# Kernel tuning notes

Hardware: AMD Instinct MI355X
Metric: run time of the kernel (lower is better)

Reference implementation:

```python
import jax, jax.numpy as jnp
import numpy as np

B, S, E, NH = 2, 2048, 1024, 4
DH = E // NH
EPS = 1e-6  # backend stabilization eps and layernorm eps


def setup_inputs() -> dict:
    key = jax.random.key(0)
    ks = jax.random.split(key, 7)
    q = jax.random.normal(ks[0], (B, S, E), jnp.float32)
    k = jax.random.normal(ks[1], (B, S, E), jnp.float32)
    v = jax.random.normal(ks[2], (B, S, E), jnp.float32)
    # Gate Dense layers: kernel zero-init in the module; use small random so the
    # math is non-trivial. Biases follow the module's inits.
    igate_kernel = 0.02 * jax.random.normal(ks[3], (3 * E, NH), jnp.float32)
    fgate_kernel = 0.02 * jax.random.normal(ks[4], (3 * E, NH), jnp.float32)
    igate_bias = 0.1 * jax.random.normal(ks[5], (NH,), jnp.float32)
    fgate_bias = jnp.linspace(3.0, 6.0, NH, dtype=jnp.float32)  # bias_linspace_init(3,6)
    outnorm_weight = jnp.ones((NH, DH), jnp.float32)
    return {
        "q": q, "k": k, "v": v,
        "igate_kernel": igate_kernel, "igate_bias": igate_bias,
        "fgate_kernel": fgate_kernel, "fgate_bias": fgate_bias,
        "outnorm_weight": outnorm_weight,
    }


def _mlstm_parallel_stabilized(q, k, v, ig, fg):
    # q,k,v: (B,NH,S,DH); ig,fg: (B,NH,S) gate pre-activations
    log_fg = jax.nn.log_sigmoid(fg)                     # (B,NH,S)
    c = jnp.cumsum(log_fg, axis=-1)                     # cumulative forget gates
    # log decay matrix: entry (i,j) = sum_{s=j+1..i} log_fg[s] = c[i]-c[j], causal
    log_fg_mat = c[..., :, None] - c[..., None, :]      # (B,NH,S,S)
    causal = jnp.tril(jnp.ones((S, S), bool))
    log_D = jnp.where(causal, log_fg_mat + ig[..., None, :], -jnp.inf)
    max_log_D = jnp.max(log_D, axis=-1, keepdims=True)  # (B,NH,S,1)
    D = jnp.exp(log_D - max_log_D)                      # stabilized decay matrix
    qk = jnp.einsum("bhsd,bhtd->bhst", q, k) / jnp.sqrt(jnp.float32(DH))
    C = qk * D                                          # (B,NH,S,S)
    normalizer = jnp.maximum(jnp.abs(jnp.sum(C, axis=-1, keepdims=True)),
                             jnp.exp(-max_log_D))
    C_norm = C / (normalizer + EPS)
    return jnp.einsum("bhst,bhtd->bhsd", C_norm, v)     # (B,NH,S,DH)


def reference(q, k, v, igate_kernel, igate_bias, fgate_kernel, fgate_bias, outnorm_weight):
    gate_in = jnp.concatenate([q, k, v], axis=-1)       # (B,S,3E)
    ig = gate_in @ igate_kernel + igate_bias            # (B,S,NH)
    fg = gate_in @ fgate_kernel + fgate_bias            # (B,S,NH)
    qh = q.reshape(B, S, NH, DH).transpose(0, 2, 1, 3)  # (B,NH,S,DH)
    kh = k.reshape(B, S, NH, DH).transpose(0, 2, 1, 3)
    vh = v.reshape(B, S, NH, DH).transpose(0, 2, 1, 3)
    h = _mlstm_parallel_stabilized(qh, kh, vh,
                                   ig.transpose(0, 2, 1), fg.transpose(0, 2, 1))
    h = h.transpose(0, 2, 1, 3)                          # (B,S,NH,DH)
    # MultiHeadLayerNorm: normalize over DH per head, weight only (no bias)
    mean = jnp.mean(h, axis=-1, keepdims=True)
    var = jnp.var(h, axis=-1, keepdims=True)
    h_norm = (h - mean) * jax.lax.rsqrt(var + EPS) * outnorm_weight
    return h_norm.reshape(B, S, E)
```

## Files before the change

kernel.cpp:

```cpp
#include <hip/hip_runtime.h>
#include <hip/hip_bf16.h>
#include <math.h>

#define B_  2
#define S_  2048
#define E_  1024
#define NH_ 4
#define DH_ 256
#define EPSF 1e-6f

typedef __attribute__((ext_vector_type(8)))  short  s16x8;
typedef __attribute__((ext_vector_type(8)))  __bf16 bf16x8;
typedef __attribute__((ext_vector_type(4)))  float  f32x4;
typedef __attribute__((ext_vector_type(16))) float  f32x16;

static __device__ __forceinline__ short f2bf(float f) {
    unsigned u = __builtin_bit_cast(unsigned, f);
    u = (u + 0x7FFFu + ((u >> 16) & 1u)) >> 16;
    return (short)u;
}

static __device__ __forceinline__ void gload16(const void* g, void* l) {
    __builtin_amdgcn_global_load_lds(
        (__attribute__((address_space(1))) void*)g,
        (__attribute__((address_space(3))) void*)l, 16, 0, 0);
}

static __device__ __host__ __forceinline__ int chunk_prefix(int N) {
    int k = N >> 3, r = N & 7;
    return 4 * k * (k + 1) + r * (k + 1);
}

__global__ void convert_qk(const float* __restrict__ q, const float* __restrict__ k,
                           short* __restrict__ qbf, short* __restrict__ kbf) {
    long gid = (long)blockIdx.x * 256 + threadIdx.x;
    const long per = (long)B_ * S_ * E_ / 8;
    const float* src = q; short* dst = qbf;
    long g2 = gid;
    if (g2 >= per) { src = k; dst = kbf; g2 -= per; }
    long flat = g2 * 8;
    int e = (int)(flat % E_);
    long bs = flat / E_;
    int s = (int)(bs % S_);
    int b = (int)(bs / S_);
    int hh = e >> 8, d = e & 255;
    const float4* p4 = (const float4*)(src + flat);
    float4 x0 = p4[0], x1 = p4[1];
    s16x8 o;
    o[0] = f2bf(x0.x); o[1] = f2bf(x0.y); o[2] = f2bf(x0.z); o[3] = f2bf(x0.w);
    o[4] = f2bf(x1.x); o[5] = f2bf(x1.y); o[6] = f2bf(x1.z); o[7] = f2bf(x1.w);
    *(s16x8*)(dst + (((long)(b * NH_ + hh) * S_ + s) * DH_ + d)) = o;
}

__global__ void transpose_v(const float* __restrict__ v, short* __restrict__ vt) {
    __shared__ short tile[64][66];
    int bid = blockIdx.x;
    int dt = bid & 3, st = (bid >> 2) & 31, hh = (bid >> 7) & 3, b = bid >> 9;
    int t = threadIdx.x;
#pragma unroll
    for (int rep = 0; rep < 16; rep++) {
        int idx = t + rep * 256;
        int ts = idx >> 6, td = idx & 63;
        float x = v[((long)b * S_ + st * 64 + ts) * E_ + hh * DH_ + dt * 64 + td];
        tile[ts][td] = f2bf(x);
    }
    __syncthreads();
    long obase = ((long)(b * NH_ + hh) * DH_ + dt * 64) * S_ + st * 64;
#pragma unroll
    for (int rep = 0; rep < 8; rep++) {
        int idx = t + rep * 256;
        int dd = idx >> 5, sp = (idx & 31) * 2;
        short2 val;
        val.x = tile[sp][dd];
        val.y = tile[sp + 1][dd];
        *(short2*)(vt + obase + (long)dd * S_ + sp) = val;
    }
}

__global__ __launch_bounds__(256)
void gates_kernel(const float* __restrict__ q, const float* __restrict__ k,
                  const float* __restrict__ v,
                  const float* __restrict__ igk, const float* __restrict__ igb,
                  const float* __restrict__ fgk, const float* __restrict__ fgb,
                  float* __restrict__ ig_ws, float* __restrict__ fg_ws) {
    int wid = threadIdx.x >> 6, lane = threadIdx.x & 63;
    int row0 = (blockIdx.x * 4 + wid) * 2;
    int b = row0 >> 11;
    int s0 = row0 & 2047;
    float accI[2][4] = {};
    float accF[2][4] = {};
    const float* srcs[3] = {q, k, v};
#pragma unroll
    for (int p = 0; p < 3; p++) {
        const float* src = srcs[p] + ((long)b * S_ + s0) * E_;
#pragma unroll
        for (int c = 0; c < 4; c++) {
            int e = c * 256 + lane * 4;
            float4 x0 = *(const float4*)(src + e);
            float4 x1 = *(const float4*)(src + E_ + e);
            const float4* wi = (const float4*)(igk + (long)(p * E_ + e) * 4);
            const float4* wf = (const float4*)(fgk + (long)(p * E_ + e) * 4);
            float xs0[4] = {x0.x, x0.y, x0.z, x0.w};
            float xs1[4] = {x1.x, x1.y, x1.z, x1.w};
#pragma unroll
            for (int j = 0; j < 4; j++) {
                float4 wij = wi[j], wfj = wf[j];
                accI[0][0] += xs0[j] * wij.x; accI[0][1] += xs0[j] * wij.y;
                accI[0][2] += xs0[j] * wij.z; accI[0][3] += xs0[j] * wij.w;
                accF[0][0] += xs0[j] * wfj.x; accF[0][1] += xs0[j] * wfj.y;
                accF[0][2] += xs0[j] * wfj.z; accF[0][3] += xs0[j] * wfj.w;
                accI[1][0] += xs1[j] * wij.x; accI[1][1] += xs1[j] * wij.y;
                accI[1][2] += xs1[j] * wij.z; accI[1][3] += xs1[j] * wij.w;
                accF[1][0] += xs1[j] * wfj.x; accF[1][1] += xs1[j] * wfj.y;
                accF[1][2] += xs1[j] * wfj.z; accF[1][3] += xs1[j] * wfj.w;
            }
        }
    }
#pragma unroll
    for (int r = 0; r < 2; r++) {
#pragma unroll
        for (int hh = 0; hh < 4; hh++) {
            float aI = accI[r][hh], aF = accF[r][hh];
            for (int m = 1; m < 64; m <<= 1) { aI += __shfl_xor(aI, m); aF += __shfl_xor(aF, m); }
            if (lane == 0) {
                ig_ws[((long)(b * NH_ + hh)) * S_ + s0 + r] = aI + igb[hh];
                fg_ws[((long)(b * NH_ + hh)) * S_ + s0 + r] = aF + fgb[hh];
            }
        }
    }
}

__global__ __launch_bounds__(256)
void scan_kernel(const float* __restrict__ ig_ws, const float* __restrict__ fg_ws,
                 float* __restrict__ c_ws, float* __restrict__ a_ws,
                 float* __restrict__ M_ws) {
    __shared__ float wsum[4], wmax[4];
    int seq = blockIdx.x;
    int tid = threadIdx.x, w = tid >> 6, lane = tid & 63;
    long base = (long)seq * S_;
    float carryC = 0.f, carryM = -INFINITY;
    for (int ch = 0; ch < S_ / 256; ch++) {
        int s = ch * 256 + tid;
        float fgv = fg_ws[base + s];
        float lf = (fgv > 0.f) ? -log1pf(expf(-fgv)) : (fgv - log1pf(expf(fgv)));
        float x = lf;
        for (int d = 1; d < 64; d <<= 1) { float t = __shfl_up(x, d); if (lane >= d) x += t; }
        if (lane == 63) wsum[w] = x;
        __syncthreads();
        float pre = carryC;
        for (int j = 0; j < w; j++) pre += wsum[j];
        float c = pre + x;
        float a = ig_ws[base + s] - c;
        float m = a;
        for (int d = 1; d < 64; d <<= 1) { float t = __shfl_up(m, d); if (lane >= d) m = fmaxf(m, t); }
        if (lane == 63) wmax[w] = m;
        __syncthreads();
        float prem = carryM;
        for (int j = 0; j < w; j++) prem = fmaxf(prem, wmax[j]);
        float M = fmaxf(prem, m);
        c_ws[base + s] = c;
        a_ws[base + s] = a;
        M_ws[base + s] = M;
        carryC += wsum[0] + wsum[1] + wsum[2] + wsum[3];
        carryM = fmaxf(fmaxf(fmaxf(carryM, wmax[0]), fmaxf(wmax[1], wmax[2])), wmax[3]);
        __syncthreads();
    }
}

__global__ __launch_bounds__(256)
void mlstm_pipe(const short* __restrict__ qbf, const short* __restrict__ kbf,
                const short* __restrict__ vt,
                const float* __restrict__ a_ws, const float* __restrict__ M_ws,
                float* __restrict__ num_ws, float* __restrict__ den_ws) {
    __shared__ __align__(16) char LDSb[139264];

    const int bid = blockIdx.x;
    const int seq = bid & 7;
    const int local = 79 - (bid >> 3);
    int qt = 0;
#pragma unroll
    for (int t = 1; t < 32; t++) if (chunk_prefix(t) <= local) qt = t;
    const int chunk = local - chunk_prefix(qt);
    const int kt0 = chunk * 8;
    const int kt1 = min(kt0 + 8, qt + 1);

    const int tid = threadIdx.x;
    const int w  = tid >> 6;
    const int rg = w & 1;
    const int ct = w >> 1;
    const int l  = tid & 63;
    const int l31 = l & 31;
    const int h5  = l >> 5;

    const long seqbase = (long)seq * S_ * DH_;
    const long gbase = (long)seq * S_;
    const int i0 = qt * 64;

    const char* kseq = (const char*)(kbf + seqbase);
    const char* vseq = (const char*)(vt + seqbase);

    int preK[8], preV[8];
#pragma unroll
    for (int i = 0; i < 8; i++) {
        int r = w * 16 + i * 2 + (l >> 5);
        preK[i] = r * 512 + (((l & 31) * 16) ^ ((r & 7) << 4));
        int d = w * 64 + i * 8 + (l >> 3);
        preV[i] = d * (S_ * 2) + (((l & 7) * 16) ^ ((d & 7) << 4));
    }

    float Mi[16];
#pragma unroll
    for (int reg = 0; reg < 16; reg++) {
        int rowL = 32 * rg + (reg & 3) + 8 * (reg >> 2) + 4 * h5;
        Mi[reg] = M_ws[gbase + i0 + rowL];
    }

    {
        short* Qlds = (short*)LDSb;
#pragma unroll
        for (int rep = 0; rep < 8; rep++) {
            int idx = tid + rep * 256;
            int r = idx >> 5, c = idx & 31;
            s16x8 val = *(const s16x8*)(qbf + seqbase + (long)(i0 + r) * DH_ + c * 8);
            int byte = (r * 512 + c * 16) ^ ((r & 7) << 4);
            *(s16x8*)((char*)Qlds + byte) = val;
        }
    }
    __syncthreads();
    bf16x8 qfrag[16];
    {
        int qrow = 32 * rg + l31;
        int qswz = (qrow & 7) << 4;
#pragma unroll
        for (int dc = 0; dc < 16; dc++)
            qfrag[dc] = *(const bf16x8*)((const char*)LDSb + ((qrow * 512 + dc * 32 + h5 * 16) ^ qswz));
    }
    __syncthreads();

    {
        const char* ks = kseq + (long)kt0 * 64 * 512;
        const char* vs = vseq + (long)kt0 * 128;
        char* kd = LDSb + w * 8192;
        char* vd = LDSb + 65536 + w * 8192;
#pragma unroll
        for (int i = 0; i < 8; i++) gload16(ks + preK[i], kd + i * 1024);
#pragma unroll
        for (int i = 0; i < 8; i++) gload16(vs + preV[i], vd + i * 1024);
    }
    __syncthreads();

    f32x16 oacc[4] = {};
    float denacc[16] = {};

    for (int kt = kt0; kt < kt1; kt++) {
        const int cur = (kt - kt0) & 1;
        const int j0 = kt * 64;

        if (kt + 1 < kt1) {
            const char* ks = kseq + (long)(kt + 1) * 64 * 512;
            const char* vs = vseq + (long)(kt + 1) * 128;
            char* kd = LDSb + (cur ^ 1) * 32768 + w * 8192;
            char* vd = LDSb + 65536 + (cur ^ 1) * 32768 + w * 8192;
#pragma unroll
            for (int i = 0; i < 8; i++) gload16(ks + preK[i], kd + i * 1024);
#pragma unroll
            for (int i = 0; i < 8; i++) gload16(vs + preV[i], vd + i * 1024);
        }

        const char* Klds  = LDSb + cur * 32768;
        const char* Vtlds = LDSb + 65536 + cur * 32768;
        char* Plds = LDSb + 131072;

        float aj = a_ws[gbase + j0 + 32 * ct + l31];

        f32x16 sacc = {};
        {
            int j = 32 * ct + l31;
            int jswz = (j & 7) << 4;
            int jbase = j * 512;
#pragma unroll
            for (int dc = 0; dc < 16; dc++) {
                bf16x8 kf = *(const bf16x8*)(Klds + ((jbase + dc * 32 + h5 * 16) ^ jswz));
                sacc = __builtin_amdgcn_mfma_f32_32x32x16_bf16(qfrag[dc], kf, sacc, 0, 0, 0);
            }
        }

        {
            int jg = j0 + 32 * ct + l31;
#pragma unroll
            for (int reg = 0; reg < 16; reg++) {
                int rowL = 32 * rg + (reg & 3) + 8 * (reg >> 2) + 4 * h5;
                float p = sacc[reg] * 0.0625f * __expf(aj - Mi[reg]);
                if (jg > i0 + rowL) p = 0.f;
                denacc[reg] += p;
                int byte = (rowL * 128 + (32 * ct + l31) * 2) ^ ((rowL & 7) << 4);
                *(short*)(Plds + byte) = f2bf(p);
            }
        }
        __syncthreads();

        bf16x8 pfrag[4];
        {
            int prow = 32 * rg + l31;
            int pswz = (prow & 7) << 4;
#pragma unroll
            for (int k4 = 0; k4 < 4; k4++)
                pfrag[k4] = *(const bf16x8*)(Plds + ((prow * 128 + k4 * 32 + h5 * 16) ^ pswz));
        }
#pragma unroll
        for (int dt = 0; dt < 4; dt++) {
            int d = 128 * ct + 32 * dt + l31;
            int dbase = d * 128, dswz = (d & 7) << 4;
#pragma unroll
            for (int k4 = 0; k4 < 4; k4++) {
                bf16x8 vf = *(const bf16x8*)(Vtlds + ((dbase + k4 * 32 + h5 * 16) ^ dswz));
                oacc[dt] = __builtin_amdgcn_mfma_f32_32x32x16_bf16(pfrag[k4], vf, oacc[dt], 0, 0, 0);
            }
        }
        __syncthreads();
    }

    const long nbase = (long)bid * 64 * 256;
#pragma unroll
    for (int reg = 0; reg < 16; reg++) {
        float dsum = denacc[reg];
        dsum += __shfl_xor(dsum, 1);
        dsum += __shfl_xor(dsum, 2);
        dsum += __shfl_xor(dsum, 4);
        dsum += __shfl_xor(dsum, 8);
        dsum += __shfl_xor(dsum, 16);
        int rowL = 32 * rg + (reg & 3) + 8 * (reg >> 2) + 4 * h5;
        if (l31 == 0) den_ws[(long)bid * 128 + ct * 64 + rowL] = dsum;
    }
#pragma unroll
    for (int dt = 0; dt < 4; dt++) {
#pragma unroll
        for (int reg = 0; reg < 16; reg++) {
            int rowL = 32 * rg + (reg & 3) + 8 * (reg >> 2) + 4 * h5;
            num_ws[nbase + (long)rowL * 256 + 128 * ct + 32 * dt + l31] = oacc[dt][reg];
        }
    }
}

__global__ __launch_bounds__(256)
void reduce_kernel(const float* __restrict__ num_ws, const float* __restrict__ den_ws,
                   const float* __restrict__ c_ws, const float* __restrict__ M_ws,
                   const float* __restrict__ onw, float* __restrict__ out) {
    const int bid = blockIdx.x;
    const int seq = bid & 7;
    const int qt = bid >> 3;
    const int h = seq & 3;
    const int b = seq >> 2;
    const int nc = (qt >> 3) + 1;
    const int lbase = chunk_prefix(qt);
    const int w = threadIdx.x >> 6;
    const int l = threadIdx.x & 63;
    const long gbase = (long)seq * S_;

    float4 w4 = *(const float4*)(onw + h * DH_ + l * 4);

    for (int rr = 0; rr < 16; rr++) {
        int row = w * 16 + rr;
        int s = qt * 64 + row;
        float4 acc = {0.f, 0.f, 0.f, 0.f};
        float dsum = 0.f;
        for (int c = 0; c < nc; c++) {
            const long cid = (long)((79 - (lbase + c)) << 3) + seq;
            const float4 p = *(const float4*)(num_ws + cid * 16384 + (long)row * 256 + l * 4);
            acc.x += p.x; acc.y += p.y; acc.z += p.z; acc.w += p.w;
            dsum += den_ws[cid * 128 + row] + den_ws[cid * 128 + 64 + row];
        }
        float lb = __expf(-c_ws[gbase + s] - M_ws[gbase + s]);
        float inv = 1.f / (fmaxf(fabsf(dsum), lb) + EPSF);
        float4 x = {acc.x * inv, acc.y * inv, acc.z * inv, acc.w * inv};
        float sum = x.x + x.y + x.z + x.w;
        sum += __shfl_xor(sum, 1); sum += __shfl_xor(sum, 2); sum += __shfl_xor(sum, 4);
        sum += __shfl_xor(sum, 8); sum += __shfl_xor(sum, 16); sum += __shfl_xor(sum, 32);
        float mean = sum * (1.f / 256.f);
        float vx = x.x - mean, vy = x.y - mean, vz = x.z - mean, vw = x.w - mean;
        float vs = vx * vx + vy * vy + vz * vz + vw * vw;
        vs += __shfl_xor(vs, 1); vs += __shfl_xor(vs, 2); vs += __shfl_xor(vs, 4);
        vs += __shfl_xor(vs, 8); vs += __shfl_xor(vs, 16); vs += __shfl_xor(vs, 32);
        float rstd = rsqrtf(vs * (1.f / 256.f) + EPSF);
        float4 o;
        o.x = vx * rstd * w4.x; o.y = vy * rstd * w4.y;
        o.z = vz * rstd * w4.z; o.w = vw * rstd * w4.w;
        *(float4*)(out + ((long)b * S_ + s) * E_ + h * DH_ + l * 4) = o;
    }
}

__global__ __launch_bounds__(256)
void mlstm_mono(const short* __restrict__ qbf, const short* __restrict__ kbf,
                const short* __restrict__ vt,
                const float* __restrict__ a_ws, const float* __restrict__ M_ws,
                const float* __restrict__ c_ws, const float* __restrict__ onw,
                float* __restrict__ out) {
    __shared__ __align__(16) short Klds[64 * 256];
    __shared__ __align__(16) short Vtlds[256 * 64];
    short* Plds = Klds;

    const int bid = blockIdx.x;
    const int seq = bid & 7;
    const int qt = bid >> 3;
    const int h = seq & 3;
    const int b = seq >> 2;
    const int tid = threadIdx.x;
    const int w = tid >> 6;
    const int l = tid & 63;
    const int l15 = l & 15;
    const int g = l >> 4;

    const long seqbase = (long)seq * S_ * DH_;
    const long gbase = (long)seq * S_;
    const int i0 = qt * 64;

    float Mi_r[4], ci_r[4];
#pragma unroll
    for (int r = 0; r < 4; r++) {
        int il = 16 * w + 4 * g + r;
        Mi_r[r] = M_ws[gbase + i0 + il];
        ci_r[r] = c_ws[gbase + i0 + il];
    }
#pragma unroll
    for (int rep = 0; rep < 8; rep++) {
        int idx = tid + rep * 256;
        int r = idx >> 5, c = idx & 31;
        s16x8 val = *(const s16x8*)(qbf + seqbase + (long)(i0 + r) * DH_ + c * 8);
        int byte = (r * 512 + c * 16) ^ ((r & 7) << 4);
        *(s16x8*)((char*)Klds + byte) = val;
    }
    __syncthreads();
    bf16x8 qfrag[8];
#pragma unroll
    for (int dc = 0; dc < 8; dc++) {
        int r = 16 * w + l15;
        int byte = (r * 512 + (8 * g + 32 * dc) * 2) ^ ((r & 7) << 4);
        qfrag[dc] = *(const bf16x8*)((const char*)Klds + byte);
    }
    __syncthreads();

    const f32x4 fzero = {0.f, 0.f, 0.f, 0.f};
    f32x4 oacc[16];
#pragma unroll
    for (int dt = 0; dt < 16; dt++) oacc[dt] = fzero;
    float den[4] = {0.f, 0.f, 0.f, 0.f};

    const int nkt = qt + 1;
    for (int kt = 0; kt < nkt; kt++) {
        const int j0 = kt * 64;
#pragma unroll
        for (int rep = 0; rep < 8; rep++) {
            int idx = tid + rep * 256;
            int r = idx >> 5, c = idx & 31;
            s16x8 val = *(const s16x8*)(kbf + seqbase + (long)(j0 + r) * DH_ + c * 8);
            int byte = (r * 512 + c * 16) ^ ((r & 7) << 4);
            *(s16x8*)((char*)Klds + byte) = val;
        }
#pragma unroll
        for (int rep = 0; rep < 8; rep++) {
            int idx = tid + rep * 256;
            int d = idx >> 3, c = idx & 7;
            s16x8 val = *(const s16x8*)(vt + seqbase + (long)d * S_ + j0 + c * 8);
            int byte = (d * 128 + c * 16) ^ ((d & 7) << 4);
            *(s16x8*)((char*)Vtlds + byte) = val;
        }
        float aj_ct[4];
#pragma unroll
        for (int ct = 0; ct < 4; ct++) aj_ct[ct] = a_ws[gbase + j0 + 16 * ct + l15];
        __syncthreads();

        f32x4 sacc[4];
#pragma unroll
        for (int ct = 0; ct < 4; ct++) sacc[ct] = fzero;
#pragma unroll
        for (int dc = 0; dc < 8; dc++) {
#pragma unroll
            for (int ct = 0; ct < 4; ct++) {
                int j = 16 * ct + l15;
                int byte = (j * 512 + (8 * g + 32 * dc) * 2) ^ ((j & 7) << 4);
                bf16x8 kf = *(const bf16x8*)((const char*)Klds + byte);
                sacc[ct] = __builtin_amdgcn_mfma_f32_16x16x32_bf16(qfrag[dc], kf, sacc[ct], 0, 0, 0);
            }
        }
        __syncthreads();

        const bool diag = (kt == qt);
#pragma unroll
        for (int ct = 0; ct < 4; ct++) {
            int jl = 16 * ct + l15;
            float aj = aj_ct[ct];
#pragma unroll
            for (int r = 0; r < 4; r++) {
                int il = 16 * w + 4 * g + r;
                float p = sacc[ct][r] * 0.0625f * __expf(aj - Mi_r[r]);
                if (diag && jl > il) p = 0.f;
                den[r] += p;
                int byte = (il * 128 + jl * 2) ^ ((il & 7) << 4);
                *(short*)((char*)Plds + byte) = f2bf(p);
            }
        }
        __syncthreads();

        bf16x8 pfrag[2];
#pragma unroll
        for (int jc = 0; jc < 2; jc++) {
            int i = 16 * w + l15;
            int byte = (i * 128 + (8 * g + 32 * jc) * 2) ^ ((i & 7) << 4);
            pfrag[jc] = *(const bf16x8*)((const char*)Plds + byte);
        }
#pragma unroll
        for (int dt = 0; dt < 16; dt++) {
#pragma unroll
            for (int jc = 0; jc < 2; jc++) {
                int d = 16 * dt + l15;
                int byte = (d * 128 + (8 * g + 32 * jc) * 2) ^ ((d & 7) << 4);
                bf16x8 vf = *(const bf16x8*)((const char*)Vtlds + byte);
                oacc[dt] = __builtin_amdgcn_mfma_f32_16x16x32_bf16(pfrag[jc], vf, oacc[dt], 0, 0, 0);
            }
        }
        __syncthreads();
    }

#pragma unroll
    for (int r = 0; r < 4; r++) {
        float dsum = den[r];
        dsum += __shfl_xor(dsum, 1);
        dsum += __shfl_xor(dsum, 2);
        dsum += __shfl_xor(dsum, 4);
        dsum += __shfl_xor(dsum, 8);
        int il = 16 * w + 4 * g + r;
        float lb = __expf(-ci_r[r] - Mi_r[r]);
        float inv = 1.f / (fmaxf(fabsf(dsum), lb) + EPSF);
        float x[16];
        float sum = 0.f;
#pragma unroll
        for (int dt = 0; dt < 16; dt++) { x[dt] = oacc[dt][r] * inv; sum += x[dt]; }
        sum += __shfl_xor(sum, 1); sum += __shfl_xor(sum, 2);
        sum += __shfl_xor(sum, 4); sum += __shfl_xor(sum, 8);
        float mean = sum * (1.f / 256.f);
        float vs = 0.f;
#pragma unroll
        for (int dt = 0; dt < 16; dt++) { float dx = x[dt] - mean; vs += dx * dx; }
        vs += __shfl_xor(vs, 1); vs += __shfl_xor(vs, 2);
        vs += __shfl_xor(vs, 4); vs += __shfl_xor(vs, 8);
        float rstd = rsqrtf(vs * (1.f / 256.f) + EPSF);
        long orow = ((long)b * S_ + i0 + il) * E_ + h * DH_;
#pragma unroll
        for (int dt = 0; dt < 16; dt++) {
            int d = 16 * dt + l15;
            out[orow + d] = (x[dt] - mean) * rstd * onw[h * DH_ + d];
        }
    }
}

extern "C" void kernel_launch(void* const* d_in, const int* in_sizes, int n_in,
                              void* d_out, int out_size, void* d_ws, size_t ws_size,
                              hipStream_t stream) {
    const float* q   = (const float*)d_in[0];
    const float* k   = (const float*)d_in[1];
    const float* v   = (const float*)d_in[2];
    const float* igk = (const float*)d_in[3];
    const float* igb = (const float*)d_in[4];
    const float* fgk = (const float*)d_in[5];
    const float* fgb = (const float*)d_in[6];
    const float* onw = (const float*)d_in[7];
    float* out = (float*)d_out;

    char* ws = (char*)d_ws;
    float* ig_ws = (float*)(ws);
    float* fg_ws = (float*)(ws + (64  << 10));
    float* c_ws  = (float*)(ws + (128 << 10));
    float* a_ws  = (float*)(ws + (192 << 10));
    float* M_ws  = (float*)(ws + (256 << 10));
    short* qbf   = (short*)(ws + (1L  << 20));
    short* kbf   = (short*)(ws + (9L  << 20));
    short* vtb   = (short*)(ws + (17L << 20));
    float* num_ws = (float*)(ws + (25L << 20));
    float* den_ws = (float*)(ws + (65L << 20));

    convert_qk  <<<4096, 256, 0, stream>>>(q, k, qbf, kbf);
    transpose_v <<<1024, 256, 0, stream>>>(v, vtb);
    gates_kernel<<<512,  256, 0, stream>>>(q, k, v, igk, igb, fgk, fgb, ig_ws, fg_ws);
    scan_kernel <<<8,    256, 0, stream>>>(ig_ws, fg_ws, c_ws, a_ws, M_ws);

    if (ws_size >= (66L << 20)) {
        mlstm_pipe  <<<640, 256, 0, stream>>>(qbf, kbf, vtb, a_ws, M_ws, num_ws, den_ws);
        reduce_kernel<<<256, 256, 0, stream>>>(num_ws, den_ws, c_ws, M_ws, onw, out);
    } else {
        mlstm_mono  <<<256, 256, 0, stream>>>(qbf, kbf, vtb, a_ws, M_ws, c_ws, onw, out);
    }
}
```

Baseline: 157.9 us.

## Fuse q/k conversion, v transpose and gate projection into one prep kernel

The separate bf16 conversion, v transpose and gate matmul kernels are merged into one launch. The gate blocks now also write the bf16 copies of q and k from the values they already loaded, so q and k are read once instead of twice. A second change doubles the reduce kernel grid so each block handles half of a 64-row tile, giving more parallelism. The cost is some extra register pressure in the gate path and a branch in the fused kernel that splits it into two kinds of blocks.

```diff
diff --git a/kernel.cpp b/kernel.cpp
--- a/kernel.cpp
+++ b/kernel.cpp
@@ -9,6 +9,7 @@
 #define DH_ 256
 #define EPSF 1e-6f
 
+typedef __attribute__((ext_vector_type(4)))  short  s16x4;
 typedef __attribute__((ext_vector_type(8)))  short  s16x8;
 typedef __attribute__((ext_vector_type(8)))  __bf16 bf16x8;
 typedef __attribute__((ext_vector_type(4)))  float  f32x4;
@@ -31,101 +32,92 @@
     return 4 * k * (k + 1) + r * (k + 1);
 }
 
-__global__ void convert_qk(const float* __restrict__ q, const float* __restrict__ k,
-                           short* __restrict__ qbf, short* __restrict__ kbf) {
-    long gid = (long)blockIdx.x * 256 + threadIdx.x;
-    const long per = (long)B_ * S_ * E_ / 8;
-    const float* src = q; short* dst = qbf;
-    long g2 = gid;
-    if (g2 >= per) { src = k; dst = kbf; g2 -= per; }
-    long flat = g2 * 8;
-    int e = (int)(flat % E_);
-    long bs = flat / E_;
-    int s = (int)(bs % S_);
-    int b = (int)(bs / S_);
-    int hh = e >> 8, d = e & 255;
-    const float4* p4 = (const float4*)(src + flat);
-    float4 x0 = p4[0], x1 = p4[1];
-    s16x8 o;
-    o[0] = f2bf(x0.x); o[1] = f2bf(x0.y); o[2] = f2bf(x0.z); o[3] = f2bf(x0.w);
-    o[4] = f2bf(x1.x); o[5] = f2bf(x1.y); o[6] = f2bf(x1.z); o[7] = f2bf(x1.w);
-    *(s16x8*)(dst + (((long)(b * NH_ + hh) * S_ + s) * DH_ + d)) = o;
-}
-
-__global__ void transpose_v(const float* __restrict__ v, short* __restrict__ vt) {
-    __shared__ short tile[64][66];
-    int bid = blockIdx.x;
-    int dt = bid & 3, st = (bid >> 2) & 31, hh = (bid >> 7) & 3, b = bid >> 9;
-    int t = threadIdx.x;
-#pragma unroll
-    for (int rep = 0; rep < 16; rep++) {
-        int idx = t + rep * 256;
-        int ts = idx >> 6, td = idx & 63;
-        float x = v[((long)b * S_ + st * 64 + ts) * E_ + hh * DH_ + dt * 64 + td];
-        tile[ts][td] = f2bf(x);
-    }
-    __syncthreads();
-    long obase = ((long)(b * NH_ + hh) * DH_ + dt * 64) * S_ + st * 64;
-#pragma unroll
-    for (int rep = 0; rep < 8; rep++) {
-        int idx = t + rep * 256;
-        int dd = idx >> 5, sp = (idx & 31) * 2;
-        short2 val;
-        val.x = tile[sp][dd];
-        val.y = tile[sp + 1][dd];
-        *(short2*)(vt + obase + (long)dd * S_ + sp) = val;
-    }
-}
-
 __global__ __launch_bounds__(256)
-void gates_kernel(const float* __restrict__ q, const float* __restrict__ k,
-                  const float* __restrict__ v,
-                  const float* __restrict__ igk, const float* __restrict__ igb,
-                  const float* __restrict__ fgk, const float* __restrict__ fgb,
-                  float* __restrict__ ig_ws, float* __restrict__ fg_ws) {
-    int wid = threadIdx.x >> 6, lane = threadIdx.x & 63;
-    int row0 = (blockIdx.x * 4 + wid) * 2;
-    int b = row0 >> 11;
-    int s0 = row0 & 2047;
-    float accI[2][4] = {};
-    float accF[2][4] = {};
-    const float* srcs[3] = {q, k, v};
-#pragma unroll
-    for (int p = 0; p < 3; p++) {
-        const float* src = srcs[p] + ((long)b * S_ + s0) * E_;
-#pragma unroll
-        for (int c = 0; c < 4; c++) {
-            int e = c * 256 + lane * 4;
-            float4 x0 = *(const float4*)(src + e);
-            float4 x1 = *(const float4*)(src + E_ + e);
-            const float4* wi = (const float4*)(igk + (long)(p * E_ + e) * 4);
-            const float4* wf = (const float4*)(fgk + (long)(p * E_ + e) * 4);
-            float xs0[4] = {x0.x, x0.y, x0.z, x0.w};
-            float xs1[4] = {x1.x, x1.y, x1.z, x1.w};
-#pragma unroll
-            for (int j = 0; j < 4; j++) {
-                float4 wij = wi[j], wfj = wf[j];
-                accI[0][0] += xs0[j] * wij.x; accI[0][1] += xs0[j] * wij.y;
-                accI[0][2] += xs0[j] * wij.z; accI[0][3] += xs0[j] * wij.w;
-                accF[0][0] += xs0[j] * wfj.x; accF[0][1] += xs0[j] * wfj.y;
-                accF[0][2] += xs0[j] * wfj.z; accF[0][3] += xs0[j] * wfj.w;
-                accI[1][0] += xs1[j] * wij.x; accI[1][1] += xs1[j] * wij.y;
-                accI[1][2] += xs1[j] * wij.z; accI[1][3] += xs1[j] * wij.w;
-                accF[1][0] += xs1[j] * wfj.x; accF[1][1] += xs1[j] * wfj.y;
-                accF[1][2] += xs1[j] * wfj.z; accF[1][3] += xs1[j] * wfj.w;
-            }
-        }
-    }
-#pragma unroll
-    for (int r = 0; r < 2; r++) {
-#pragma unroll
-        for (int hh = 0; hh < 4; hh++) {
-            float aI = accI[r][hh], aF = accF[r][hh];
-            for (int m = 1; m < 64; m <<= 1) { aI += __shfl_xor(aI, m); aF += __shfl_xor(aF, m); }
-            if (lane == 0) {
-                ig_ws[((long)(b * NH_ + hh)) * S_ + s0 + r] = aI + igb[hh];
-                fg_ws[((long)(b * NH_ + hh)) * S_ + s0 + r] = aF + fgb[hh];
-            }
+void prep_kernel(const float* __restrict__ q, const float* __restrict__ k,
+                 const float* __restrict__ v,
+                 const float* __restrict__ igk, const float* __restrict__ igb,
+                 const float* __restrict__ fgk, const float* __restrict__ fgb,
+                 short* __restrict__ qbf, short* __restrict__ kbf,
+                 short* __restrict__ vt,
+                 float* __restrict__ ig_ws, float* __restrict__ fg_ws) {
+    const int bid = blockIdx.x;
+    if (bid < 512) {
+        int wid = threadIdx.x >> 6, lane = threadIdx.x & 63;
+        int row0 = (bid * 4 + wid) * 2;
+        int b = row0 >> 11;
+        int s0 = row0 & 2047;
+        float accI[2][4] = {};
+        float accF[2][4] = {};
+        const float* srcs[3] = {q, k, v};
+        short* dsts[2] = {qbf, kbf};
+#pragma unroll
+        for (int p = 0; p < 3; p++) {
+            const float* src = srcs[p] + ((long)b * S_ + s0) * E_;
+#pragma unroll
+            for (int c = 0; c < 4; c++) {
+                int e = c * 256 + lane * 4;
+                float4 x0 = *(const float4*)(src + e);
+                float4 x1 = *(const float4*)(src + E_ + e);
+                if (p < 2) {
+                    s16x4 o0, o1;
+                    o0[0] = f2bf(x0.x); o0[1] = f2bf(x0.y); o0[2] = f2bf(x0.z); o0[3] = f2bf(x0.w);
+                    o1[0] = f2bf(x1.x); o1[1] = f2bf(x1.y); o1[2] = f2bf(x1.z); o1[3] = f2bf(x1.w);
+                    long db = ((long)(b * NH_ + c) * S_ + s0) * DH_ + lane * 4;
+                    *(s16x4*)(dsts[p] + db) = o0;
+                    *(s16x4*)(dsts[p] + db + DH_) = o1;
+                }
+                const float4* wi = (const float4*)(igk + (long)(p * E_ + e) * 4);
+                const float4* wf = (const float4*)(fgk + (long)(p * E_ + e) * 4);
+                float xs0[4] = {x0.x, x0.y, x0.z, x0.w};
+                float xs1[4] = {x1.x, x1.y, x1.z, x1.w};
+#pragma unroll
+                for (int j = 0; j < 4; j++) {
+                    float4 wij = wi[j], wfj = wf[j];
+                    accI[0][0] += xs0[j] * wij.x; accI[0][1] += xs0[j] * wij.y;
+                    accI[0][2] += xs0[j] * wij.z; accI[0][3] += xs0[j] * wij.w;
+                    accF[0][0] += xs0[j] * wfj.x; accF[0][1] += xs0[j] * wfj.y;
+                    accF[0][2] += xs0[j] * wfj.z; accF[0][3] += xs0[j] * wfj.w;
+                    accI[1][0] += xs1[j] * wij.x; accI[1][1] += xs1[j] * wij.y;
+                    accI[1][2] += xs1[j] * wij.z; accI[1][3] += xs1[j] * wij.w;
+                    accF[1][0] += xs1[j] * wfj.x; accF[1][1] += xs1[j] * wfj.y;
+                    accF[1][2] += xs1[j] * wfj.z; accF[1][3] += xs1[j] * wfj.w;
+                }
+            }
+        }
+#pragma unroll
+        for (int r = 0; r < 2; r++) {
+#pragma unroll
+            for (int hh = 0; hh < 4; hh++) {
+                float aI = accI[r][hh], aF = accF[r][hh];
+                for (int m = 1; m < 64; m <<= 1) { aI += __shfl_xor(aI, m); aF += __shfl_xor(aF, m); }
+                if (lane == 0) {
+                    ig_ws[((long)(b * NH_ + hh)) * S_ + s0 + r] = aI + igb[hh];
+                    fg_ws[((long)(b * NH_ + hh)) * S_ + s0 + r] = aF + fgb[hh];
+                }
+            }
+        }
+    } else {
+        __shared__ short tile[64][66];
+        int b2 = bid - 512;
+        int dt = b2 & 3, st = (b2 >> 2) & 31, hh = (b2 >> 7) & 3, b = b2 >> 9;
+        int t = threadIdx.x;
+#pragma unroll
+        for (int rep = 0; rep < 16; rep++) {
+            int idx = t + rep * 256;
+            int ts = idx >> 6, td = idx & 63;
+            float x = v[((long)b * S_ + st * 64 + ts) * E_ + hh * DH_ + dt * 64 + td];
+            tile[ts][td] = f2bf(x);
+        }
+        __syncthreads();
+        long obase = ((long)(b * NH_ + hh) * DH_ + dt * 64) * S_ + st * 64;
+#pragma unroll
+        for (int rep = 0; rep < 8; rep++) {
+            int idx = t + rep * 256;
+            int dd = idx >> 5, sp = (idx & 31) * 2;
+            short2 val;
+            val.x = tile[sp][dd];
+            val.y = tile[sp + 1][dd];
+            *(short2*)(vt + obase + (long)dd * S_ + sp) = val;
         }
     }
 }
@@ -348,7 +340,9 @@
                    const float* __restrict__ onw, float* __restrict__ out) {
     const int bid = blockIdx.x;
     const int seq = bid & 7;
-    const int qt = bid >> 3;
+    const int qh = bid >> 3;
+    const int qt = qh >> 1;
+    const int half = qh & 1;
     const int h = seq & 3;
     const int b = seq >> 2;
     const int nc = (qt >> 3) + 1;
@@ -359,8 +353,8 @@
 
     float4 w4 = *(const float4*)(onw + h * DH_ + l * 4);
 
-    for (int rr = 0; rr < 16; rr++) {
-        int row = w * 16 + rr;
+    for (int rr = 0; rr < 8; rr++) {
+        int row = half * 32 + w * 8 + rr;
         int s = qt * 64 + row;
         float4 acc = {0.f, 0.f, 0.f, 0.f};
         float dsum = 0.f;
@@ -578,14 +572,13 @@
     float* num_ws = (float*)(ws + (25L << 20));
     float* den_ws = (float*)(ws + (65L << 20));
 
-    convert_qk  <<<4096, 256, 0, stream>>>(q, k, qbf, kbf);
-    transpose_v <<<1024, 256, 0, stream>>>(v, vtb);
-    gates_kernel<<<512,  256, 0, stream>>>(q, k, v, igk, igb, fgk, fgb, ig_ws, fg_ws);
-    scan_kernel <<<8,    256, 0, stream>>>(ig_ws, fg_ws, c_ws, a_ws, M_ws);
+    prep_kernel<<<1536, 256, 0, stream>>>(q, k, v, igk, igb, fgk, fgb,
+                                          qbf, kbf, vtb, ig_ws, fg_ws);
+    scan_kernel<<<8, 256, 0, stream>>>(ig_ws, fg_ws, c_ws, a_ws, M_ws);
 
     if (ws_size >= (66L << 20)) {
         mlstm_pipe  <<<640, 256, 0, stream>>>(qbf, kbf, vtb, a_ws, M_ws, num_ws, den_ws);
-        reduce_kernel<<<256, 256, 0, stream>>>(num_ws, den_ws, c_ws, M_ws, onw, out);
+        reduce_kernel<<<512, 256, 0, stream>>>(num_ws, den_ws, c_ws, M_ws, onw, out);
     } else {
         mlstm_mono  <<<256, 256, 0, stream>>>(qbf, kbf, vtb, a_ws, M_ws, c_ws, onw, out);
     }
```

Measured after the change: 151.1 us. -4.4%, faster.
